# Optimization experiments

Hardware: AMD Instinct MI355X
Metric: run time of the kernel (lower is better)

The kernel has to match this reference:

```python
import jax, jax.numpy as jnp
import numpy as np

B, C, H, W = 4, 8, 1024, 1024
R = 1  # stencil radius


def setup_inputs() -> dict:
    key = jax.random.key(0)
    k1, k2, k3 = jax.random.split(key, 3)
    x = jax.random.normal(k1, (B, C + 1, H, W), dtype=jnp.float32)
    rand = jax.random.uniform(k2, (B, C, H, W), dtype=jnp.float32)
    dropout_rand = jax.random.uniform(k3, (H, W), dtype=jnp.float32)
    # cross-shaped nearest-neighbour kernel: row R and col R = 1, center = 0
    Rk = 2 * R + 1
    k = np.zeros((1, C, Rk, Rk), dtype=np.float32)
    k[:, :, R, :] = 1.0
    k[:, :, :, R] = 1.0
    k[:, :, R, R] = 0.0
    nn_kernel = jnp.asarray(k)
    return {"x": x, "rand": rand, "dropout_rand": dropout_rand, "nn_kernel": nn_kernel}


def reference(x, rand, dropout_rand, nn_kernel):
    C_ = nn_kernel.shape[1]
    R_ = (nn_kernel.shape[2] - 1) // 2
    s = x[:, :C_]          # [B, C, H, W] spins
    b = x[:, -1:]          # [B, 1, H, W] inverse temperature
    # circular pad then valid conv == circular convolution with cross stencil
    s_pad = jnp.pad(s, ((0, 0), (0, 0), (R_, R_), (R_, R_)), mode="wrap")
    Js = jax.lax.conv_general_dilated(
        s_pad, nn_kernel, window_strides=(1, 1), padding="VALID",
        dimension_numbers=("NCHW", "OIHW", "NCHW"))  # [B, 1, H, W]
    delta_e = 2.0 * s * Js                      # broadcast over channels
    p = jnp.where(delta_e <= 0, jnp.ones_like(s), jnp.exp(-delta_e * b))
    dropout_mask = (dropout_rand > 0.5)[None, None]  # [1,1,H,W]
    flip = 1.0 - 2.0 * ((rand < p) & dropout_mask).astype(s.dtype)
    return jnp.concatenate([s * flip, b], axis=1)
```

## Files before the change

### kernel.cpp

```cpp
#include <hip/hip_runtime.h>
#include <math.h>

#define HH 1024
#define WW 1024
#define BB 4
#define CC 8

struct double4_t { double x, y, z, w; };

__device__ __forceinline__ float decide(float s, double Js, double bb, float r, float d) {
    double de = (2.0 * (double)s) * Js;
    bool flip;
    if (de <= 0.0) {
        flip = true;
    } else {
        double p = exp(-de * bb);
        flip = ((double)r < p);
    }
    flip = flip && (d > 0.5f);
    return flip ? -s : s;
}

__global__ __launch_bounds__(256) void ising_sweep(
    const float* __restrict__ x,
    const float* __restrict__ rnd,
    const float* __restrict__ drop,
    float* __restrict__ out)
{
    const int i  = blockIdx.x;
    const int b  = blockIdx.y;
    const int j0 = threadIdx.x * 4;

    const int im1 = (i == 0)      ? (HH - 1) : (i - 1);
    const int ip1 = (i == HH - 1) ? 0        : (i + 1);
    const int jl  = (j0 == 0)        ? (WW - 1) : (j0 - 1);
    const int jr  = (j0 + 4 == WW)   ? 0        : (j0 + 4);

    const size_t plane = (size_t)HH * WW;
    const float* xb = x + (size_t)b * 9 * plane;

    float4 sreg[CC];
    double4_t Js = {0.0, 0.0, 0.0, 0.0};

    #pragma unroll
    for (int c = 0; c < CC; ++c) {
        const float* xc = xb + (size_t)c * plane;
        const float4 up = *(const float4*)(xc + (size_t)im1 * WW + j0);
        const float4 dn = *(const float4*)(xc + (size_t)ip1 * WW + j0);
        const float4 ce = *(const float4*)(xc + (size_t)i   * WW + j0);
        const float  lf = xc[(size_t)i * WW + jl];
        const float  rt = xc[(size_t)i * WW + jr];
        sreg[c] = ce;
        Js.x += (double)up.x + (double)lf   + (double)ce.y + (double)dn.x;
        Js.y += (double)up.y + (double)ce.x + (double)ce.z + (double)dn.y;
        Js.z += (double)up.z + (double)ce.y + (double)ce.w + (double)dn.z;
        Js.w += (double)up.w + (double)ce.z + (double)rt   + (double)dn.w;
    }

    const float4 bv = *(const float4*)(xb + (size_t)8 * plane + (size_t)i * WW + j0);
    const float4 dr = *(const float4*)(drop + (size_t)i * WW + j0);
    const double4_t bd = {(double)bv.x, (double)bv.y, (double)bv.z, (double)bv.w};

    const float* rb = rnd + (size_t)b * CC * plane;
    float*       ob = out + (size_t)b * 9 * plane;

    #pragma unroll
    for (int c = 0; c < CC; ++c) {
        const float4 rv = *(const float4*)(rb + (size_t)c * plane + (size_t)i * WW + j0);
        float4 o;
        o.x = decide(sreg[c].x, Js.x, bd.x, rv.x, dr.x);
        o.y = decide(sreg[c].y, Js.y, bd.y, rv.y, dr.y);
        o.z = decide(sreg[c].z, Js.z, bd.z, rv.z, dr.z);
        o.w = decide(sreg[c].w, Js.w, bd.w, rv.w, dr.w);
        *(float4*)(ob + (size_t)c * plane + (size_t)i * WW + j0) = o;
    }
    *(float4*)(ob + (size_t)8 * plane + (size_t)i * WW + j0) = bv;
}

extern "C" void kernel_launch(void* const* d_in, const int* in_sizes, int n_in,
                              void* d_out, int out_size, void* d_ws, size_t ws_size,
                              hipStream_t stream) {
    const float* x    = (const float*)d_in[0];
    const float* rnd  = (const float*)d_in[1];
    const float* drop = (const float*)d_in[2];
    float* out = (float*)d_out;

    dim3 grid(HH, BB);
    dim3 block(WW / 4);
    ising_sweep<<<grid, block, 0, stream>>>(x, rnd, drop, out);
}
```

Before: 360.5 us.

## Use float fast-exp with double fallback, shuffle halos, nontemporal stores

Replaces the per-element double-precision exp with a float __expf plus an error band, and falls back to the exact double computation only when the random value lies inside that band. Left and right halo values now come from wavefront shuffles, with global loads only at lane edges. Spin values are reloaded in the second loop instead of kept in registers, the launch bounds add an occupancy hint, and the rand reads and output writes use nontemporal hints. These target the double-precision ALU cost and register pressure, at the cost of relying on the error band to keep results identical to the original.

New measurement: 510.0 us. 1.41x slower.

```diff
diff --git a/kernel.cpp b/kernel.cpp
--- a/kernel.cpp
+++ b/kernel.cpp
@@ -6,75 +6,98 @@
 #define BB 4
 #define CC 8
 
-struct double4_t { double x, y, z, w; };
+typedef float v4f __attribute__((ext_vector_type(4)));
 
-__device__ __forceinline__ float decide(float s, double Js, double bb, float r, float d) {
-    double de = (2.0 * (double)s) * Js;
+__device__ __forceinline__ float decide(float s, float tt, float Jsf, double Js,
+                                        float bb, float r, bool keep) {
+    const float argf = s * tt;
     bool flip;
-    if (de <= 0.0) {
+    if ((s * Jsf <= 0.0f) | (argf >= 0.0f)) {
         flip = true;
     } else {
-        double p = exp(-de * bb);
-        flip = ((double)r < p);
+        const float pe  = __expf(argf);
+        const float err = fmaf(fabsf(argf), 6.0e-7f, 2.0e-6f) * pe;
+        if (r < pe - err)      flip = true;
+        else if (r > pe + err) flip = false;
+        else {
+            double de = (2.0 * (double)s) * Js;
+            flip = (de <= 0.0) || ((double)r < exp(-de * (double)bb));
+        }
     }
-    flip = flip && (d > 0.5f);
-    return flip ? -s : s;
+    return (flip & keep) ? -s : s;
 }
 
-__global__ __launch_bounds__(256) void ising_sweep(
+__global__ __launch_bounds__(256, 6) void ising_sweep(
     const float* __restrict__ x,
     const float* __restrict__ rnd,
     const float* __restrict__ drop,
     float* __restrict__ out)
 {
-    const int i  = blockIdx.x;
-    const int b  = blockIdx.y;
-    const int j0 = threadIdx.x * 4;
+    const int i    = blockIdx.x;
+    const int b    = blockIdx.y;
+    const int t    = threadIdx.x;
+    const int j0   = t * 4;
+    const int lane = t & 63;
 
     const int im1 = (i == 0)      ? (HH - 1) : (i - 1);
     const int ip1 = (i == HH - 1) ? 0        : (i + 1);
-    const int jl  = (j0 == 0)        ? (WW - 1) : (j0 - 1);
-    const int jr  = (j0 + 4 == WW)   ? 0        : (j0 + 4);
+    const int jl  = (j0 == 0)      ? (WW - 1) : (j0 - 1);
+    const int jr  = (j0 + 4 == WW) ? 0        : (j0 + 4);
+    const bool edge = (lane == 0) | (lane == 63);
+    const int  je   = (lane == 0) ? jl : jr;
 
     const size_t plane = (size_t)HH * WW;
     const float* xb = x + (size_t)b * 9 * plane;
+    const size_t rowu = (size_t)im1 * WW + j0;
+    const size_t rowd = (size_t)ip1 * WW + j0;
+    const size_t rowc = (size_t)i   * WW + j0;
+    const size_t rowe = (size_t)i   * WW + je;
 
-    float4 sreg[CC];
-    double4_t Js = {0.0, 0.0, 0.0, 0.0};
+    double Jx = 0.0, Jy = 0.0, Jz = 0.0, Jw = 0.0;
 
     #pragma unroll
     for (int c = 0; c < CC; ++c) {
         const float* xc = xb + (size_t)c * plane;
-        const float4 up = *(const float4*)(xc + (size_t)im1 * WW + j0);
-        const float4 dn = *(const float4*)(xc + (size_t)ip1 * WW + j0);
-        const float4 ce = *(const float4*)(xc + (size_t)i   * WW + j0);
-        const float  lf = xc[(size_t)i * WW + jl];
-        const float  rt = xc[(size_t)i * WW + jr];
-        sreg[c] = ce;
-        Js.x += (double)up.x + (double)lf   + (double)ce.y + (double)dn.x;
-        Js.y += (double)up.y + (double)ce.x + (double)ce.z + (double)dn.y;
-        Js.z += (double)up.z + (double)ce.y + (double)ce.w + (double)dn.z;
-        Js.w += (double)up.w + (double)ce.z + (double)rt   + (double)dn.w;
+        const v4f up = *(const v4f*)(xc + rowu);
+        const v4f dn = *(const v4f*)(xc + rowd);
+        const v4f ce = *(const v4f*)(xc + rowc);
+        float lf = __shfl_up(ce.w, 1);
+        float rt = __shfl_down(ce.x, 1);
+        if (edge) {
+            const float ev = xc[rowe];
+            if (lane == 0) lf = ev; else rt = ev;
+        }
+        Jx += (double)up.x + (double)lf   + (double)ce.y + (double)dn.x;
+        Jy += (double)up.y + (double)ce.x + (double)ce.z + (double)dn.y;
+        Jz += (double)up.z + (double)ce.y + (double)ce.w + (double)dn.z;
+        Jw += (double)up.w + (double)ce.z + (double)rt   + (double)dn.w;
     }
 
-    const float4 bv = *(const float4*)(xb + (size_t)8 * plane + (size_t)i * WW + j0);
-    const float4 dr = *(const float4*)(drop + (size_t)i * WW + j0);
-    const double4_t bd = {(double)bv.x, (double)bv.y, (double)bv.z, (double)bv.w};
+    const v4f bv = *(const v4f*)(xb + (size_t)8 * plane + rowc);
+    const v4f dr = *(const v4f*)(drop + rowc);
+    const bool kx = dr.x > 0.5f, ky = dr.y > 0.5f, kz = dr.z > 0.5f, kw = dr.w > 0.5f;
+
+    const float ttx = -2.0f * (float)(Jx * (double)bv.x);
+    const float tty = -2.0f * (float)(Jy * (double)bv.y);
+    const float ttz = -2.0f * (float)(Jz * (double)bv.z);
+    const float ttw = -2.0f * (float)(Jw * (double)bv.w);
+    const float Jxf = (float)Jx, Jyf = (float)Jy, Jzf = (float)Jz, Jwf = (float)Jw;
 
     const float* rb = rnd + (size_t)b * CC * plane;
     float*       ob = out + (size_t)b * 9 * plane;
 
     #pragma unroll
     for (int c = 0; c < CC; ++c) {
-        const float4 rv = *(const float4*)(rb + (size_t)c * plane + (size_t)i * WW + j0);
-        float4 o;
-        o.x = decide(sreg[c].x, Js.x, bd.x, rv.x, dr.x);
-        o.y = decide(sreg[c].y, Js.y, bd.y, rv.y, dr.y);
-        o.z = decide(sreg[c].z, Js.z, bd.z, rv.z, dr.z);
-        o.w = decide(sreg[c].w, Js.w, bd.w, rv.w, dr.w);
-        *(float4*)(ob + (size_t)c * plane + (size_t)i * WW + j0) = o;
+        const v4f sv = *(const v4f*)(xb + (size_t)c * plane + rowc);
+        const v4f rv = __builtin_nontemporal_load((const v4f*)(rb + (size_t)c * plane + rowc));
+        v4f o;
+        o.x = decide(sv.x, ttx, Jxf, Jx, bv.x, rv.x, kx);
+        o.y = decide(sv.y, tty, Jyf, Jy, bv.y, rv.y, ky);
+        o.z = decide(sv.z, ttz, Jzf, Jz, bv.z, rv.z, kz);
+        o.w = decide(sv.w, ttw, Jwf, Jw, bv.w, rv.w, kw);
+        __builtin_nontemporal_store(o, (v4f*)(ob + (size_t)c * plane + rowc));
     }
-    *(float4*)(ob + (size_t)8 * plane + (size_t)i * WW + j0) = bv;
+    __builtin_nontemporal_store(bv, (v4f*)(ob + (size_t)8 * plane + rowc));
 }
 
 extern "C" void kernel_launch(void* const* d_in, const int* in_sizes, int n_in,
```
